# Optimization experiments

Hardware: AMD Instinct MI355X
Metric: run time of the kernel (lower is better)

The kernel has to match this reference:

```python
import jax, jax.numpy as jnp
import numpy as np

BN_EPS = 1e-5
NEG_SLOPE = 0.01  # F.leaky_relu default
MASK_VAL = 1e8


def setup_inputs() -> dict:
    key = jax.random.key(0)
    k1, k2, k3, k4 = jax.random.split(key, 4)
    B, H, D, L = 8, 128, 512, 128
    out_dim, inner = 128, 3 * 128  # inner_dim = (order*support_len + 1) * c_in = 3*H
    x = jax.random.normal(k1, (B, H, D, L), dtype=jnp.float32)
    d_x = jax.random.normal(k2, (B, H, D, L - 1), dtype=jnp.float32)
    conv_w = jax.random.normal(k3, (out_dim, inner), dtype=jnp.float32) * 0.05
    conv_b = jax.random.normal(k4, (out_dim,), dtype=jnp.float32) * 0.05
    bn_gamma = jnp.ones((out_dim,), dtype=jnp.float32)
    bn_beta = jnp.zeros((out_dim,), dtype=jnp.float32)
    return {"x": x, "d_x": d_x, "conv_w": conv_w, "conv_b": conv_b,
            "bn_gamma": bn_gamma, "bn_beta": bn_beta, "max_len": L}


def reference(x, d_x, conv_w, conv_b, bn_gamma, bn_beta, max_len):
    B, H, D, L = x.shape
    V = 2 * D  # node dimension of the pooled graph

    # --- gather-based index pooling ---
    idx = jnp.argmax(jnp.abs(d_x), axis=-1, keepdims=True)        # [B,H,D,1]
    pool_idx = jnp.concatenate([idx, idx + 1], axis=-1)           # [B,H,D,2]
    pv = jnp.take_along_axis(x, pool_idx, axis=-1)                # [B,H,D,2]
    pv = pv.reshape(B, H, V)                                      # [B,H,2D]

    # --- masked-softmax adjacency ---
    adj = jnp.einsum('bhv,bhw->bvw', pv, pv) / V                  # [B,2D,2D]
    eye = jnp.eye(V, dtype=x.dtype)
    adj_masked = adj - eye * MASK_VAL
    pooling_adj = jax.nn.softmax(jax.nn.leaky_relu(adj_masked, NEG_SLOPE), axis=-1) + eye

    # --- GCN: order-2 nconv message passing + 1x1 conv + batchnorm (training stats) ---
    x0 = pv                                                       # [B,H,V] (L=1 squeezed)
    x1 = jnp.einsum('bcv,bvw->bcw', x0, pooling_adj)
    x2 = jnp.einsum('bcv,bvw->bcw', x1, pooling_adj)
    h = jnp.concatenate([x0, x1, x2], axis=1)                     # [B,3H,V]
    h = jnp.einsum('biv,oi->bov', h, conv_w) + conv_b[None, :, None]  # [B,H,V]

    mean = jnp.mean(h, axis=(0, 2), keepdims=True)
    var = jnp.var(h, axis=(0, 2), keepdims=True)
    h = bn_gamma[None, :, None] * (h - mean) * jax.lax.rsqrt(var + BN_EPS) + bn_beta[None, :, None]
    # dropout: identity at inference

    # --- output reshuffle: [B,H,2D] -> [B,2H,D] ---
    res = h.reshape(B, H, D, 2)
    res = jnp.transpose(res, (0, 2, 3, 1))                        # [B,D,2,H]
    res = res.reshape(B, D, 2 * H)
    return jnp.swapaxes(res, -1, -2)                              # [B,2H,D]
```

## Files before the change

kernel.cpp:

```cpp
#include <hip/hip_runtime.h>
#include <cstdint>

#define L_ 128

using bf16   = __bf16;
using bf16x2 = __attribute__((ext_vector_type(2))) __bf16;
using bf16x4 = __attribute__((ext_vector_type(4))) __bf16;
using bf16x8 = __attribute__((ext_vector_type(8))) __bf16;
using f32x4  = __attribute__((ext_vector_type(4))) float;

#define MFMA_B16(a, b, c) __builtin_amdgcn_mfma_f32_16x16x32_bf16((a), (b), (c), 0, 0, 0)

__global__ __launch_bounds__(256) void k_pool(const float* __restrict__ x,
                                              const float* __restrict__ dx,
                                              bf16* __restrict__ pvb) {
  const int64_t gt = (int64_t)blockIdx.x * 256 + threadIdx.x;
  const int64_t row = gt >> 2;
  const int j = (int)(gt & 3);
  const float* rp = dx + row * 127;

  float bv = -1.0f;
  int bi = 0;
#pragma unroll
  for (int i = 0; i < 8; ++i) {
    int base = 16 * i + 4 * j;
    if (base > 123) base = 123;
    float4 v = *(const float4*)(rp + base);
    float a = fabsf(v.x);
    if (a > bv) { bv = a; bi = base; }
    a = fabsf(v.y);
    if (a > bv) { bv = a; bi = base + 1; }
    a = fabsf(v.z);
    if (a > bv) { bv = a; bi = base + 2; }
    a = fabsf(v.w);
    if (a > bv) { bv = a; bi = base + 3; }
  }
#pragma unroll
  for (int off = 1; off <= 2; off <<= 1) {
    float ov = __shfl_xor(bv, off, 64);
    int   oi = __shfl_xor(bi, off, 64);
    if (ov > bv || (ov == bv && oi < bi)) { bv = ov; bi = oi; }
  }
  if (j == 0) {
    const float* xr = x + row * L_;
    bf16x2 o;
    o[0] = (bf16)xr[bi];
    o[1] = (bf16)xr[bi + 1];
    int64_t bh = row >> 9;
    int d = (int)(row & 511);
    *(bf16x2*)(pvb + (bh << 10) + 2 * d) = o;
  }
}

__global__ __launch_bounds__(256) void k_tr(const bf16* __restrict__ pvb,
                                            bf16* __restrict__ XT) {
  __shared__ bf16 t[64][66];
  const int b  = blockIdx.x >> 5;
  const int hb = (blockIdx.x >> 4) & 1;
  const int vb = blockIdx.x & 15;
  const int tid = threadIdx.x;
  const bf16* src = pvb + ((int64_t)b << 17) + (int64_t)(hb << 6) * 1024 + (vb << 6);
#pragma unroll
  for (int i = 0; i < 16; ++i) {
    int e = i * 256 + tid;
    int r = e >> 6, c = e & 63;
    t[r][c] = src[(int64_t)r * 1024 + c];
  }
  __syncthreads();
  bf16* dst = XT + ((int64_t)b << 10) * 384 + (int64_t)(vb << 6) * 384 + (hb << 6);
#pragma unroll
  for (int i = 0; i < 16; ++i) {
    int e = i * 256 + tid;
    int vr = e >> 6, hc = e & 63;
    dst[(int64_t)vr * 384 + hc] = t[hc][vr];
  }
}

__global__ __launch_bounds__(256) void k_adj(const bf16* __restrict__ XT,
                                             bf16* __restrict__ AT) {
  const int b  = blockIdx.x >> 6;
  const int vb = blockIdx.x & 63;
  const int tid = threadIdx.x, lane = tid & 63, wid = tid >> 6;
  const int g = lane >> 4, rl = lane & 15;
  const bf16* Xb = XT + (int64_t)b * 1024 * 384;

  __shared__ bf16 lsA[16 * 128];
  __shared__ float redmax[16][4];
  __shared__ float redsum[16][4];

  {
    int row = tid >> 4, c8 = tid & 15;
    bf16x8 v = *(const bf16x8*)(Xb + (int64_t)(vb * 16 + row) * 384 + c8 * 8);
    *(bf16x8*)((char*)lsA + row * 256 + ((c8 ^ (row & 7)) << 4)) = v;
  }
  __syncthreads();

  bf16x8 af[4];
#pragma unroll
  for (int ks = 0; ks < 4; ++ks)
    af[ks] = *(const bf16x8*)((char*)lsA + rl * 256 + ((((ks << 2) | g) ^ (rl & 7)) << 4));

  f32x4 acc[16];
  f32x4 zero = {0.f, 0.f, 0.f, 0.f};
#pragma unroll
  for (int t = 0; t < 16; ++t) acc[t] = zero;

  const int nbase = wid * 256;
#pragma unroll
  for (int t = 0; t < 16; ++t) {
    const bf16* bp = Xb + (int64_t)(nbase + t * 16 + rl) * 384 + g * 8;
#pragma unroll
    for (int ks = 0; ks < 4; ++ks) {
      bf16x8 bfr = *(const bf16x8*)(bp + ks * 32);
      acc[t] = MFMA_B16(af[ks], bfr, acc[t]);
    }
  }

  const int vg0 = vb * 16 + g * 4;
  float rmax[4] = {-1e30f, -1e30f, -1e30f, -1e30f};
#pragma unroll
  for (int t = 0; t < 16; ++t) {
    int n = nbase + t * 16 + rl;
#pragma unroll
    for (int r = 0; r < 4; ++r) {
      float a = acc[t][r] * (1.0f / 1024.0f);
      if (n == vg0 + r) a -= 1e8f;
      a = (a > 0.f) ? a : 0.01f * a;
      acc[t][r] = a;
      rmax[r] = fmaxf(rmax[r], a);
    }
  }
#pragma unroll
  for (int r = 0; r < 4; ++r)
#pragma unroll
    for (int off = 1; off < 16; off <<= 1)
      rmax[r] = fmaxf(rmax[r], __shfl_xor(rmax[r], off, 64));
  if (rl == 0)
#pragma unroll
    for (int r = 0; r < 4; ++r) redmax[g * 4 + r][wid] = rmax[r];
  __syncthreads();
#pragma unroll
  for (int r = 0; r < 4; ++r)
    rmax[r] = fmaxf(fmaxf(redmax[g * 4 + r][0], redmax[g * 4 + r][1]),
                    fmaxf(redmax[g * 4 + r][2], redmax[g * 4 + r][3]));

  float rsum[4] = {0.f, 0.f, 0.f, 0.f};
#pragma unroll
  for (int t = 0; t < 16; ++t)
#pragma unroll
    for (int r = 0; r < 4; ++r) {
      float e = __expf(acc[t][r] - rmax[r]);
      acc[t][r] = e;
      rsum[r] += e;
    }
#pragma unroll
  for (int r = 0; r < 4; ++r)
#pragma unroll
    for (int off = 1; off < 16; off <<= 1) rsum[r] += __shfl_xor(rsum[r], off, 64);
  if (rl == 0)
#pragma unroll
    for (int r = 0; r < 4; ++r) redsum[g * 4 + r][wid] = rsum[r];
  __syncthreads();
#pragma unroll
  for (int r = 0; r < 4; ++r) {
    float s = redsum[g * 4 + r][0] + redsum[g * 4 + r][1] +
              redsum[g * 4 + r][2] + redsum[g * 4 + r][3];
    rsum[r] = 1.0f / s;
  }

  bf16* ATb = AT + ((int64_t)b << 20);
#pragma unroll
  for (int t = 0; t < 16; ++t) {
    int n = nbase + t * 16 + rl;
    bf16x4 o;
#pragma unroll
    for (int r = 0; r < 4; ++r) {
      float v = acc[t][r] * rsum[r] + ((n == vg0 + r) ? 1.0f : 0.0f);
      o[r] = (bf16)v;
    }
    *(bf16x4*)(ATb + (int64_t)n * 1024 + vb * 16 + g * 4) = o;
  }
}

template <int WRITE_ROW, int TCOL>
__global__ __launch_bounds__(256) void k_gemm(const bf16* __restrict__ Xa,
                                              const bf16* __restrict__ AT,
                                              bf16* __restrict__ Yrow,
                                              bf16* __restrict__ XT) {
  const int b  = blockIdx.x >> 4;
  const int n0 = (blockIdx.x & 15) << 6;
  const int tid = threadIdx.x, lane = tid & 63, wid = tid >> 6;
  const int g = lane >> 4, rl = lane & 15;
  const bf16* Xb = Xa + ((int64_t)b << 17);
  const bf16* Ab = AT + ((int64_t)b << 20);

  __shared__ bf16 lsA[128 * 64];
  __shared__ bf16 lsB[64 * 64];

  const int wbase = tid & ~63;

  auto STAGE = [&](int ks) {
    const int k0 = ks << 6;
#pragma unroll
    for (int i = 0; i < 4; ++i) {
      int f = (i << 8) + tid;
      int row = f >> 3;
      int sc8 = (f & 7) ^ (row & 7);
      const bf16* src = Xb + (int64_t)row * 1024 + k0 + (sc8 << 3);
      char* dst = (char*)lsA + (((i << 8) + wbase) << 4);
      __builtin_amdgcn_global_load_lds(
          (const __attribute__((address_space(1))) void*)src,
          (__attribute__((address_space(3))) void*)dst, 16, 0, 0);
    }
#pragma unroll
    for (int i = 0; i < 2; ++i) {
      int f = (i << 8) + tid;
      int row = f >> 3;
      int sc8 = (f & 7) ^ (row & 7);
      const bf16* src = Ab + (int64_t)(n0 + row) * 1024 + k0 + (sc8 << 3);
      char* dst = (char*)lsB + (((i << 8) + wbase) << 4);
      __builtin_amdgcn_global_load_lds(
          (const __attribute__((address_space(1))) void*)src,
          (__attribute__((address_space(3))) void*)dst, 16, 0, 0);
    }
  };

  f32x4 acc[2][4];
  f32x4 zero = {0.f, 0.f, 0.f, 0.f};
#pragma unroll
  for (int mi = 0; mi < 2; ++mi)
#pragma unroll
    for (int ni = 0; ni < 4; ++ni) acc[mi][ni] = zero;

  STAGE(0);
  __syncthreads();

  for (int ks = 0; ks < 16; ++ks) {
    bf16x8 afr[2][2], bfr[4][2];
#pragma unroll
    for (int mi = 0; mi < 2; ++mi)
#pragma unroll
      for (int ku = 0; ku < 2; ++ku) {
        int row = wid * 32 + mi * 16 + rl;
        afr[mi][ku] = *(const bf16x8*)((char*)lsA + row * 128 +
                                       ((((ku << 2) | g) ^ (rl & 7)) << 4));
      }
#pragma unroll
    for (int ni = 0; ni < 4; ++ni)
#pragma unroll
      for (int ku = 0; ku < 2; ++ku) {
        int row = ni * 16 + rl;
        bfr[ni][ku] = *(const bf16x8*)((char*)lsB + row * 128 +
                                       ((((ku << 2) | g) ^ (rl & 7)) << 4));
      }
    __syncthreads();
    if (ks < 15) STAGE(ks + 1);
#pragma unroll
    for (int ku = 0; ku < 2; ++ku)
#pragma unroll
      for (int mi = 0; mi < 2; ++mi)
#pragma unroll
        for (int ni = 0; ni < 4; ++ni)
          acc[mi][ni] = MFMA_B16(afr[mi][ku], bfr[ni][ku], acc[mi][ni]);
    __syncthreads();
  }

#pragma unroll
  for (int mi = 0; mi < 2; ++mi)
#pragma unroll
    for (int ni = 0; ni < 4; ++ni) {
      int c0 = wid * 32 + mi * 16 + g * 4;
      int w  = n0 + ni * 16 + rl;
      if (WRITE_ROW) {
#pragma unroll
        for (int q = 0; q < 4; ++q)
          Yrow[((int64_t)b << 17) + (int64_t)(c0 + q) * 1024 + w] = (bf16)acc[mi][ni][q];
      }
      bf16x4 o;
#pragma unroll
      for (int q = 0; q < 4; ++q) o[q] = (bf16)acc[mi][ni][q];
      *(bf16x4*)(XT + ((int64_t)b * 1024 + w) * 384 + TCOL + c0) = o;
    }
}

__global__ __launch_bounds__(256) void k_conv(const float* __restrict__ W,
                                              const bf16* __restrict__ XT,
                                              const float* __restrict__ bias,
                                              float* __restrict__ h) {
  const int b  = blockIdx.x >> 4;
  const int n0 = (blockIdx.x & 15) << 6;
  const int tid = threadIdx.x, lane = tid & 63, wid = tid >> 6;
  const int g = lane >> 4, rl = lane & 15;
  const bf16* Xb = XT + (int64_t)b * 1024 * 384;

  __shared__ bf16 lsA[128 * 64];
  __shared__ bf16 lsB[64 * 64];

  bf16x8 stA[4], stB[2];

  auto LOAD = [&](int ks) {
    const int k0 = ks << 6;
#pragma unroll
    for (int i = 0; i < 4; ++i) {
      int f = i * 256 + tid;
      int row = f >> 3, c8 = f & 7;
      const float* wp = W + (int64_t)row * 384 + k0 + c8 * 8;
      float4 a0 = *(const float4*)(wp);
      float4 a1 = *(const float4*)(wp + 4);
      bf16x8 r;
      r[0] = (bf16)a0.x; r[1] = (bf16)a0.y; r[2] = (bf16)a0.z; r[3] = (bf16)a0.w;
      r[4] = (bf16)a1.x; r[5] = (bf16)a1.y; r[6] = (bf16)a1.z; r[7] = (bf16)a1.w;
      stA[i] = r;
    }
#pragma unroll
    for (int i = 0; i < 2; ++i) {
      int f = i * 256 + tid;
      int row = f >> 3, c8 = f & 7;
      stB[i] = *(const bf16x8*)(Xb + (int64_t)(n0 + row) * 384 + k0 + c8 * 8);
    }
  };
  auto WRITE = [&]() {
#pragma unroll
    for (int i = 0; i < 4; ++i) {
      int f = i * 256 + tid;
      int row = f >> 3, c8 = f & 7;
      *(bf16x8*)((char*)lsA + row * 128 + ((c8 ^ (row & 7)) << 4)) = stA[i];
    }
#pragma unroll
    for (int i = 0; i < 2; ++i) {
      int f = i * 256 + tid;
      int row = f >> 3, c8 = f & 7;
      *(bf16x8*)((char*)lsB + row * 128 + ((c8 ^ (row & 7)) << 4)) = stB[i];
    }
  };

  f32x4 acc[2][4];
  f32x4 zero = {0.f, 0.f, 0.f, 0.f};
#pragma unroll
  for (int mi = 0; mi < 2; ++mi)
#pragma unroll
    for (int ni = 0; ni < 4; ++ni) acc[mi][ni] = zero;

  LOAD(0);
  WRITE();
  __syncthreads();

  for (int ks = 0; ks < 6; ++ks) {
    bf16x8 afr[2][2], bfr[4][2];
#pragma unroll
    for (int mi = 0; mi < 2; ++mi)
#pragma unroll
      for (int ku = 0; ku < 2; ++ku) {
        int row = wid * 32 + mi * 16 + rl;
        afr[mi][ku] = *(const bf16x8*)((char*)lsA + row * 128 +
                                       ((((ku << 2) | g) ^ (rl & 7)) << 4));
      }
#pragma unroll
    for (int ni = 0; ni < 4; ++ni)
#pragma unroll
      for (int ku = 0; ku < 2; ++ku) {
        int row = ni * 16 + rl;
        bfr[ni][ku] = *(const bf16x8*)((char*)lsB + row * 128 +
                                       ((((ku << 2) | g) ^ (rl & 7)) << 4));
      }
    if (ks < 5) LOAD(ks + 1);
    __syncthreads();
    if (ks < 5) WRITE();
#pragma unroll
    for (int ku = 0; ku < 2; ++ku)
#pragma unroll
      for (int mi = 0; mi < 2; ++mi)
#pragma unroll
        for (int ni = 0; ni < 4; ++ni)
          acc[mi][ni] = MFMA_B16(afr[mi][ku], bfr[ni][ku], acc[mi][ni]);
    __syncthreads();
  }

#pragma unroll
  for (int mi = 0; mi < 2; ++mi)
#pragma unroll
    for (int ni = 0; ni < 4; ++ni) {
      int c0 = wid * 32 + mi * 16 + g * 4;
      int w  = n0 + ni * 16 + rl;
#pragma unroll
      for (int q = 0; q < 4; ++q)
        h[((int64_t)(b * 128 + c0 + q) << 10) + w] = acc[mi][ni][q] + bias[c0 + q];
    }
}

__global__ __launch_bounds__(256) void k_statsout(const float* __restrict__ hpre,
                                                  const float* __restrict__ gamma,
                                                  const float* __restrict__ beta,
                                                  float* __restrict__ out) {
  const int o = blockIdx.x;
  const int tid = threadIdx.x;
  float s = 0.f, s2 = 0.f;
  for (int e = tid; e < 8192; e += 256) {
    int bb = e >> 10, v = e & 1023;
    float val = hpre[((int64_t)(bb * 128 + o) << 10) + v];
    s += val;
    s2 = fmaf(val, val, s2);
  }
#pragma unroll
  for (int off = 1; off < 64; off <<= 1) {
    s  += __shfl_xor(s, off, 64);
    s2 += __shfl_xor(s2, off, 64);
  }
  __shared__ float rs[4], rs2[4];
  __shared__ float scsh[2];
  int lane = tid & 63, wid = tid >> 6;
  if (lane == 0) { rs[wid] = s; rs2[wid] = s2; }
  __syncthreads();
  if (tid == 0) {
    float S  = rs[0] + rs[1] + rs[2] + rs[3];
    float S2 = rs2[0] + rs2[1] + rs2[2] + rs2[3];
    float mean = S * (1.0f / 8192.0f);
    float var  = S2 * (1.0f / 8192.0f) - mean * mean;
    float istd = rsqrtf(var + 1e-5f);
    float scale = gamma[o] * istd;
    scsh[0] = scale;
    scsh[1] = beta[o] - mean * scale;
  }
  __syncthreads();
  const float sc = scsh[0], sh = scsh[1];
  for (int q = tid; q < 8192; q += 256) {
    int b  = q >> 10;
    int pd = q & 1023;
    int p  = pd >> 9;
    int d  = pd & 511;
    float val = hpre[(((int64_t)(b * 128 + o)) << 10) + 2 * d + p];
    out[(((int64_t)(b * 256 + p * 128 + o)) << 9) + d] = fmaf(val, sc, sh);
  }
}

extern "C" void kernel_launch(void* const* d_in, const int* in_sizes, int n_in,
                              void* d_out, int out_size, void* d_ws, size_t ws_size,
                              hipStream_t stream) {
  const float* x     = (const float*)d_in[0];
  const float* dx    = (const float*)d_in[1];
  const float* W     = (const float*)d_in[2];
  const float* cb    = (const float*)d_in[3];
  const float* gamma = (const float*)d_in[4];
  const float* beta  = (const float*)d_in[5];

  char* ws = (char*)d_ws;
  bf16*   XcatT = (bf16*)(ws);
  bf16*   AT    = (bf16*)(ws + 6291456);
  bf16*   pvb   = (bf16*)(ws + 23068672);
  bf16*   x1b   = (bf16*)(ws + 25165824);
  float*  h     = (float*)(ws + 27361280);
  float* out    = (float*)d_out;

  k_pool<<<8192, 256, 0, stream>>>(x, dx, pvb);
  k_tr<<<256, 256, 0, stream>>>(pvb, XcatT);
  k_adj<<<512, 256, 0, stream>>>(XcatT, AT);
  k_gemm<1, 128><<<128, 256, 0, stream>>>(pvb, AT, x1b, XcatT);
  k_gemm<0, 256><<<128, 256, 0, stream>>>(x1b, AT, nullptr, XcatT);
  k_conv<<<128, 256, 0, stream>>>(W, XcatT, cb, h);
  k_statsout<<<128, 256, 0, stream>>>(h, gamma, beta, out);
}
```

Baseline: 140.9 us.

## Stage d_x rows through LDS with coalesced double-buffered loads in pooling kernel

The argmax pooling kernel now has each wave load 8 contiguous rows of d_x (1016 floats) with fully coalesced float4 loads into a per-wave LDS double buffer. The next chunk's global load is overlapped with the argmax and gather on the current chunk. Each wave handles 128 rows, so the grid shrinks from 8192 to 1024 blocks. The goal is to fix the poorly coalesced per-row float4 reads caused by the 127-float row stride. In exchange it adds LDS traffic, fewer blocks in flight, and hand-written waitcnt and wave-barrier synchronisation.

```diff
diff --git a/kernel.cpp b/kernel.cpp
--- a/kernel.cpp
+++ b/kernel.cpp
@@ -14,41 +14,76 @@
 __global__ __launch_bounds__(256) void k_pool(const float* __restrict__ x,
                                               const float* __restrict__ dx,
                                               bf16* __restrict__ pvb) {
-  const int64_t gt = (int64_t)blockIdx.x * 256 + threadIdx.x;
-  const int64_t row = gt >> 2;
-  const int j = (int)(gt & 3);
-  const float* rp = dx + row * 127;
-
-  float bv = -1.0f;
-  int bi = 0;
-#pragma unroll
-  for (int i = 0; i < 8; ++i) {
-    int base = 16 * i + 4 * j;
-    if (base > 123) base = 123;
-    float4 v = *(const float4*)(rp + base);
-    float a = fabsf(v.x);
-    if (a > bv) { bv = a; bi = base; }
-    a = fabsf(v.y);
-    if (a > bv) { bv = a; bi = base + 1; }
-    a = fabsf(v.z);
-    if (a > bv) { bv = a; bi = base + 2; }
-    a = fabsf(v.w);
-    if (a > bv) { bv = a; bi = base + 3; }
-  }
-#pragma unroll
-  for (int off = 1; off <= 2; off <<= 1) {
-    float ov = __shfl_xor(bv, off, 64);
-    int   oi = __shfl_xor(bi, off, 64);
-    if (ov > bv || (ov == bv && oi < bi)) { bv = ov; bi = oi; }
-  }
-  if (j == 0) {
-    const float* xr = x + row * L_;
-    bf16x2 o;
-    o[0] = (bf16)xr[bi];
-    o[1] = (bf16)xr[bi + 1];
-    int64_t bh = row >> 9;
-    int d = (int)(row & 511);
-    *(bf16x2*)(pvb + (bh << 10) + 2 * d) = o;
+  __shared__ float4 lds[8][256];
+  const int tid = threadIdx.x;
+  const int lane = tid & 63;
+  const int w = tid >> 6;
+  const int k = lane & 7;
+  const int r = lane >> 3;
+  const int64_t wrow0 = ((int64_t)blockIdx.x * 4 + w) * 128;
+  float4* const wbuf = &lds[w * 2][0];
+
+  float4 st[4];
+  auto LOADG = [&](int c) {
+    const float* src = dx + (wrow0 + (int64_t)c * 8) * 127;
+#pragma unroll
+    for (int i = 0; i < 4; ++i) {
+      int fi = lane + (i << 6);
+      if (fi < 254) st[i] = *(const float4*)(src + 4 * fi);
+    }
+  };
+  auto DSW = [&](int buf) {
+    float4* dstb = wbuf + buf * 256;
+#pragma unroll
+    for (int i = 0; i < 4; ++i) {
+      int fi = lane + (i << 6);
+      if (fi < 254) dstb[fi] = st[i];
+    }
+  };
+
+  LOADG(0);
+  DSW(0);
+  int cur = 0;
+  for (int c = 0; c < 16; ++c) {
+    asm volatile("s_waitcnt lgkmcnt(0)" ::: "memory");
+    __builtin_amdgcn_wave_barrier();
+    const float* rowp = (const float*)(wbuf + cur * 256) + r * 127;
+    float bv = -1.0f;
+    int bi = 0;
+#pragma unroll
+    for (int m = 0; m < 16; ++m) {
+      int col = (m << 3) + k;
+      if (col < 127) {
+        float a = fabsf(rowp[col]);
+        if (a > bv) { bv = a; bi = col; }
+      }
+    }
+#pragma unroll
+    for (int off = 1; off <= 4; off <<= 1) {
+      float ov = __shfl_xor(bv, off, 64);
+      int   oi = __shfl_xor(bi, off, 64);
+      if (ov > bv || (ov == bv && oi < bi)) { bv = ov; bi = oi; }
+    }
+    const int64_t row = wrow0 + (int64_t)c * 8 + r;
+    float gx = 0.f, gy = 0.f;
+    if (k == 0) {
+      const float* xr = x + row * L_;
+      gx = xr[bi];
+      gy = xr[bi + 1];
+    }
+    if (c < 15) LOADG(c + 1);
+    if (k == 0) {
+      bf16x2 o;
+      o[0] = (bf16)gx;
+      o[1] = (bf16)gy;
+      int64_t bh = row >> 9;
+      int d = (int)(row & 511);
+      *(bf16x2*)(pvb + (bh << 10) + 2 * d) = o;
+    }
+    if (c < 15) DSW(cur ^ 1);
+    __builtin_amdgcn_wave_barrier();
+    asm volatile("" ::: "memory");
+    cur ^= 1;
   }
 }
 
@@ -451,7 +486,7 @@
   float*  h     = (float*)(ws + 27361280);
   float* out    = (float*)d_out;
 
-  k_pool<<<8192, 256, 0, stream>>>(x, dx, pvb);
+  k_pool<<<1024, 256, 0, stream>>>(x, dx, pvb);
   k_tr<<<256, 256, 0, stream>>>(pvb, XcatT);
   k_adj<<<512, 256, 0, stream>>>(XcatT, AT);
   k_gemm<1, 128><<<128, 256, 0, stream>>>(pvb, AT, x1b, XcatT);
```

New measurement: 205.7 us. 46.0% more time.
